# Kernel optimization log

Hardware: AMD Instinct MI355X
Metric: run time of the kernel (lower is better)

Reference implementation:

```python
import jax, jax.numpy as jnp
import numpy as np

IMG_W = 256; IMG_H = 256; N_PTS = 320
MIN_DEPTH = 3.0; MAX_DEPTH = 9.0
NDC_EXTENT = 1.0; SCALING = 0.1; EPS = 1e-10


def setup_inputs() -> dict:
    key = jax.random.key(0)
    k1, k2, k3 = jax.random.split(key, 3)
    B, S = 1, 256
    image3d = jax.random.uniform(k1, (B, 1, S, S, S), dtype=jnp.float32)
    # random proper rotation via QR
    A = jax.random.normal(k2, (B, 3, 3), dtype=jnp.float32)
    Q, _ = jnp.linalg.qr(A)
    det = jnp.linalg.det(Q)
    R = Q * det[:, None, None]  # det(+1) for 3x3
    # camera ~6 world units in front of volume center (depth range 3..9)
    T = jnp.concatenate([0.1 * jax.random.normal(k3, (B, 2), dtype=jnp.float32),
                         jnp.full((B, 1), 6.0, jnp.float32)], axis=1)
    focal = jnp.full((B,), 4.0, jnp.float32)
    return {"image3d": image3d, "R": R, "T": T, "focal": focal}


def _trilinear(vol, pts):
    # vol: (C,D,H,W); pts: (N,3) xyz local coords in [-1,1]
    # grid_sample semantics: trilinear, align_corners=True, zero padding
    C, D, H, W = vol.shape
    gx = (pts[:, 0] + 1.0) * 0.5 * (W - 1)
    gy = (pts[:, 1] + 1.0) * 0.5 * (H - 1)
    gz = (pts[:, 2] + 1.0) * 0.5 * (D - 1)
    x0 = jnp.floor(gx); y0 = jnp.floor(gy); z0 = jnp.floor(gz)
    fx = gx - x0; fy = gy - y0; fz = gz - z0
    vol_flat = vol.reshape(C, D * H * W)
    out = jnp.zeros((C, pts.shape[0]), vol.dtype)
    for dz in (0, 1):
        wz = fz if dz else 1.0 - fz
        cz = z0 + dz
        for dy in (0, 1):
            wy = fy if dy else 1.0 - fy
            cy = y0 + dy
            for dx in (0, 1):
                wx = fx if dx else 1.0 - fx
                cx = x0 + dx
                valid = ((cx >= 0) & (cx <= W - 1) & (cy >= 0) & (cy <= H - 1)
                         & (cz >= 0) & (cz <= D - 1)).astype(vol.dtype)
                idx = ((jnp.clip(cz, 0, D - 1) * H + jnp.clip(cy, 0, H - 1)) * W
                       + jnp.clip(cx, 0, W - 1)).astype(jnp.int32)
                w = wx * wy * wz * valid
                out = out + vol_flat[:, idx] * w[None, :]
    return out


def _render(image3d, R, T, focal):
    B, C, D, H, W = image3d.shape
    voxel_size = 2.0 * NDC_EXTENT / max(C, D)  # shape = max(C, D) in original
    # Volumes local<->world scale per axis (pytorch3d): voxel_size*(size-1)/2
    scale = jnp.array([voxel_size * (W - 1) / 2.0,
                       voxel_size * (H - 1) / 2.0,
                       voxel_size * (D - 1) / 2.0], jnp.float32)
    # NDCMultinomialRaysampler pixel grid (pytorch3d: +x left, +y up, decreasing)
    xs = jnp.linspace(1.0 - 1.0 / IMG_W, -1.0 + 1.0 / IMG_W, IMG_W)
    ys = jnp.linspace(1.0 - 1.0 / IMG_H, -1.0 + 1.0 / IMG_H, IMG_H)
    depths = jnp.linspace(MIN_DEPTH, MAX_DEPTH, N_PTS).astype(jnp.float32)
    gy, gx = jnp.meshgrid(ys, xs, indexing="ij")  # (Hi,Wi)

    # channel 0: gray volume (features); channel 1: ones (density support)
    vol2 = jnp.concatenate([image3d[:, :1], jnp.ones_like(image3d[:, :1])], axis=1)

    def one(volC, Rb, Tb, fb):
        # unproject NDC pixels at each depth: cam pt = (x*d/f, y*d/f, d)
        cx = gx[:, :, None] * depths[None, None, :] / fb
        cy = gy[:, :, None] * depths[None, None, :] / fb
        cz = jnp.broadcast_to(depths, (IMG_H, IMG_W, N_PTS))
        cam = jnp.stack([cx, cy, cz], -1).reshape(-1, 3)       # (N,3)
        world = (cam - Tb) @ Rb.T                              # X_view = X_world @ R + T
        local = world / scale
        return _trilinear(volC, local)                          # (2,N)

    samp = jax.vmap(one)(vol2, R, T, focal)                     # (B,2,N)
    samp = samp.reshape(B, 2, IMG_H, IMG_W, N_PTS)
    gray = samp[:, 0]
    dens = SCALING * samp[:, 1]

    # EmissionAbsorptionRaymarcher (shifted cumprod, shift=1)
    cp = jnp.cumprod((1.0 + EPS) - dens, axis=-1)
    absorption = jnp.concatenate([jnp.ones_like(cp[..., :1]), cp[..., :-1]], axis=-1)
    weights = dens * absorption
    feat = jnp.sum(weights * gray, axis=-1)                     # RGB channels are equal
    opacity = 1.0 - jnp.prod(1.0 - dens, axis=-1)

    # RGBA (B,Hi,Wi,4) -> permute(0,3,2,1) -> mean over channel = (3*feat+alpha)/4
    screen = (3.0 * feat + opacity) / 4.0
    screen = jnp.transpose(screen, (0, 2, 1))[:, None]          # (B,1,Wi,Hi)

    # norm_type='standardized': normalized(standardized(x)), torch std is unbiased
    s = (screen - screen.mean()) / (jnp.std(screen, ddof=1) + 1e-8)
    return (s - s.min() + 1e-8) / (s.max() - s.min() + 1e-8)


def reference(image3d, R, T, focal):
    return _render(image3d, R, T, focal)
```

## Files before the change

### kernel.cpp

```cpp
#include <hip/hip_runtime.h>
#include <math.h>

#define IMG    256
#define NPTS   320
#define CHUNKS 8
#define SPC    40
#define NBLK   1024

__global__ __launch_bounds__(512)
void xray_render(const float* __restrict__ vol,
                 const float* __restrict__ Rm,
                 const float* __restrict__ Tv,
                 const float* __restrict__ fc,
                 float* __restrict__ outv,
                 float* __restrict__ partials)
{
    const int tid = threadIdx.x;
    const int p   = tid & 63;
    const int c   = tid >> 6;
    const int w   = (blockIdx.x << 3) + (p & 7);
    const int h   = (blockIdx.y << 3) + (p >> 3);

    const float f   = fc[0];
    const float r00 = Rm[0], r01 = Rm[1], r02 = Rm[2];
    const float r10 = Rm[3], r11 = Rm[4], r12 = Rm[5];
    const float r20 = Rm[6], r21 = Rm[7], r22 = Rm[8];
    const float t0  = Tv[0], t1  = Tv[1], t2  = Tv[2];

    const float invf = 1.0f / f;
    const float px = 0.99609375f - (float)w * 0.0078125f;
    const float py = 0.99609375f - (float)h * 0.0078125f;
    const float dcx = px * invf, dcy = py * invf;

    const float dwx = r00*dcx + r01*dcy + r02;
    const float dwy = r10*dcx + r11*dcy + r12;
    const float dwz = r20*dcx + r21*dcy + r22;
    const float ox  = -(r00*t0 + r01*t1 + r02*t2);
    const float oy  = -(r10*t0 + r11*t1 + r12*t2);
    const float oz  = -(r20*t0 + r21*t1 + r22*t2);

    const float g0x = fmaf(384.0f, dwx, fmaf(128.0f, ox, 127.5f));
    const float g0y = fmaf(384.0f, dwy, fmaf(128.0f, oy, 127.5f));
    const float g0z = fmaf(384.0f, dwz, fmaf(128.0f, oz, 127.5f));
    const float K   = 768.0f / 319.0f;
    const float gsx = K*dwx, gsy = K*dwy, gsz = K*dwz;

    float raylo = -1e30f, rayhi = 1e30f;
    float inlo  = -1e30f, inhi  = 1e30f;
    {
        const float g0a[3] = {g0x, g0y, g0z};
        const float gsa[3] = {gsx, gsy, gsz};
        #pragma unroll
        for (int a = 0; a < 3; ++a) {
            const float g0 = g0a[a], gs = gsa[a];
            if (fabsf(gs) > 1e-6f) {
                const float r = 1.0f / gs;
                const float u = (-1.0f  - g0) * r;
                const float v = (256.0f - g0) * r;
                raylo = fmaxf(raylo, fminf(u, v));
                rayhi = fminf(rayhi, fmaxf(u, v));
                const float s = (0.001f   - g0) * r;
                const float t = (254.999f - g0) * r;
                inlo = fmaxf(inlo, fminf(s, t));
                inhi = fminf(inhi, fmaxf(s, t));
            } else {
                if (!(g0 > -1.0f && g0 < 256.0f))        { raylo = 1e30f; rayhi = -1e30f; }
                if (!(g0 > 0.001f && g0 < 254.999f))     { inlo  = 1e30f; inhi  = -1e30f; }
            }
        }
    }
    const float c0f = (float)(c * SPC);
    const float c1f = c0f + (float)(SPC - 1);
    float a0 = fminf(fmaxf(fmaxf(raylo - 1.0f, c0f), 0.0f),  400.0f);
    float a1 = fminf(fmaxf(fminf(rayhi + 1.0f, c1f), -1.0f), 400.0f);
    const int i0 = (int)ceilf(a0);
    const int i1 = (int)floorf(a1);
    float b0 = fminf(fmaxf(inlo, (float)i0), 401.0f);
    float b1 = fmaxf(fminf(inhi, (float)i1), -2.0f);
    const int jLo = (int)ceilf(b0);
    const int jHi = (int)floorf(b1);

    float feat = 0.0f, Tc = 1.0f;

    auto bstep = [&](int i) {
        const float fi = (float)i;
        const float gx = fmaf(fi, gsx, g0x);
        const float gy = fmaf(fi, gsy, g0y);
        const float gz = fmaf(fi, gsz, g0z);
        const float xf = floorf(gx), yf = floorf(gy), zf = floorf(gz);
        const float fx = gx - xf, fy = gy - yf, fz = gz - zf;
        const int ix = (int)xf, iy = (int)yf, iz = (int)zf;
        const float wx0 = (ix >= 0  && ix <= 255) ? (1.0f - fx) : 0.0f;
        const float wx1 = (ix >= -1 && ix <= 254) ? fx          : 0.0f;
        const float wy0 = (iy >= 0  && iy <= 255) ? (1.0f - fy) : 0.0f;
        const float wy1 = (iy >= -1 && iy <= 254) ? fy          : 0.0f;
        const float wz0 = (iz >= 0  && iz <= 255) ? (1.0f - fz) : 0.0f;
        const float wz1 = (iz >= -1 && iz <= 254) ? fz          : 0.0f;
        const float cov = (wx0 + wx1) * (wy0 + wy1) * (wz0 + wz1);
        if (cov > 0.0f) {
            const int x0 = min(max(ix, 0), 255),   x1 = min(max(ix + 1, 0), 255);
            const int y0 = min(max(iy, 0), 255),   y1 = min(max(iy + 1, 0), 255);
            const int z0 = min(max(iz, 0), 255),   z1 = min(max(iz + 1, 0), 255);
            const float* bz0 = vol + (z0 << 16);
            const float* bz1 = vol + (z1 << 16);
            const int ry0 = y0 << 8, ry1 = y1 << 8;
            const float s0 = (bz0[ry0 + x0]*wx0 + bz0[ry0 + x1]*wx1) * wy0
                           + (bz0[ry1 + x0]*wx0 + bz0[ry1 + x1]*wx1) * wy1;
            const float s1 = (bz1[ry0 + x0]*wx0 + bz1[ry0 + x1]*wx1) * wy0
                           + (bz1[ry1 + x0]*wx0 + bz1[ry1 + x1]*wx1) * wy1;
            const float gray = s0 * wz0 + s1 * wz1;
            const float dens = 0.1f * cov;
            feat = fmaf(dens * Tc, gray, feat);
            Tc *= (1.0f - dens);
        }
    };

    if (jLo <= jHi) {
        for (int i = i0; i < jLo; ++i) bstep(i);

        #pragma unroll 4
        for (int i = jLo; i <= jHi; ++i) {
            const float fi = (float)i;
            const float gx = fmaf(fi, gsx, g0x);
            const float gy = fmaf(fi, gsy, g0y);
            const float gz = fmaf(fi, gsz, g0z);
            const int ix = (int)gx;
            const int iy = (int)gy;
            const int iz = (int)gz;
            const float fx = gx - (float)ix;
            const float fy = gy - (float)iy;
            const float fz = gz - (float)iz;
            const float* b = vol + ((iz << 16) + (iy << 8) + ix);
            const float v000 = b[0],     v001 = b[1];
            const float v010 = b[256],   v011 = b[257];
            const float v100 = b[65536], v101 = b[65537];
            const float v110 = b[65792], v111 = b[65793];
            const float c00 = fmaf(fx, v001 - v000, v000);
            const float c01 = fmaf(fx, v011 - v010, v010);
            const float c10 = fmaf(fx, v101 - v100, v100);
            const float c11 = fmaf(fx, v111 - v110, v110);
            const float d0  = fmaf(fy, c01 - c00, c00);
            const float d1  = fmaf(fy, c11 - c10, c10);
            const float gray = fmaf(fz, d1 - d0, d0);
            feat = fmaf(0.1f * Tc, gray, feat);
            Tc *= 0.9f;
        }

        for (int i = jHi + 1; i <= i1; ++i) bstep(i);
    } else {
        for (int i = i0; i <= i1; ++i) bstep(i);
    }

    __shared__ float sf[CHUNKS][64];
    __shared__ float sT[CHUNKS][64];
    sf[c][p] = feat; sT[c][p] = Tc;
    __syncthreads();

    if (tid < 64) {
        float F = sf[CHUNKS - 1][p];
        #pragma unroll
        for (int j = CHUNKS - 2; j >= 0; --j) F = fmaf(sT[j][p], F, sf[j][p]);
        float PR = sT[0][p];
        #pragma unroll
        for (int j = 1; j < CHUNKS; ++j) PR *= sT[j][p];

        const float screen = fmaf(3.0f, F, 1.0f - PR) * 0.25f;
        outv[(w << 8) + h] = screen;

        float s = screen, s2 = screen * screen, mn = screen, mx = screen;
        #pragma unroll
        for (int o = 32; o; o >>= 1) {
            s  += __shfl_xor(s,  o);
            s2 += __shfl_xor(s2, o);
            mn  = fminf(mn, __shfl_xor(mn, o));
            mx  = fmaxf(mx, __shfl_xor(mx, o));
        }
        if (p == 0) {
            const int bid = (blockIdx.y << 5) + blockIdx.x;
            partials[bid * 4 + 0] = s;
            partials[bid * 4 + 1] = s2;
            partials[bid * 4 + 2] = mn;
            partials[bid * 4 + 3] = mx;
        }
    }
}

__global__ __launch_bounds__(256)
void xray_normalize(float* __restrict__ outv, const float* __restrict__ partials)
{
    const int t = threadIdx.x;
    double s = 0.0, s2 = 0.0;
    float mn = 1e30f, mx = -1e30f;
    #pragma unroll
    for (int j = 0; j < NBLK / 256; ++j) {
        const int idx = (j * 256 + t) * 4;
        s  += (double)partials[idx + 0];
        s2 += (double)partials[idx + 1];
        mn  = fminf(mn, partials[idx + 2]);
        mx  = fmaxf(mx, partials[idx + 3]);
    }
    #pragma unroll
    for (int o = 32; o; o >>= 1) {
        s  += __shfl_xor(s,  o);
        s2 += __shfl_xor(s2, o);
        mn  = fminf(mn, __shfl_xor(mn, o));
        mx  = fmaxf(mx, __shfl_xor(mx, o));
    }
    __shared__ double ls[4], ls2[4];
    __shared__ float  lmn[4], lmx[4];
    __shared__ float  soff, sinv;
    const int wid = t >> 6, lane = t & 63;
    if (lane == 0) { ls[wid] = s; ls2[wid] = s2; lmn[wid] = mn; lmx[wid] = mx; }
    __syncthreads();
    if (t == 0) {
        const double S  = ls[0] + ls[1] + ls[2] + ls[3];
        const double S2 = ls2[0] + ls2[1] + ls2[2] + ls2[3];
        const float MN = fminf(fminf(lmn[0], lmn[1]), fminf(lmn[2], lmn[3]));
        const float MX = fmaxf(fmaxf(lmx[0], lmx[1]), fmaxf(lmx[2], lmx[3]));
        double var = (S2 - S * S / 65536.0) / 65535.0;
        if (var < 0.0) var = 0.0;
        const double sdp = sqrt(var) + 1e-8;
        const float off = MN - (float)(1e-8 * sdp);
        soff = off;
        sinv = 1.0f / (MX - off);
    }
    __syncthreads();
    const int i = blockIdx.x * 256 + t;
    outv[i] = (outv[i] - soff) * sinv;
}

extern "C" void kernel_launch(void* const* d_in, const int* in_sizes, int n_in,
                              void* d_out, int out_size, void* d_ws, size_t ws_size,
                              hipStream_t stream)
{
    const float* vol = (const float*)d_in[0];
    const float* Rm  = (const float*)d_in[1];
    const float* Tv  = (const float*)d_in[2];
    const float* fc  = (const float*)d_in[3];
    float* outv = (float*)d_out;
    float* partials = (float*)d_ws;

    dim3 grid(IMG / 8, IMG / 8);
    xray_render<<<grid, 512, 0, stream>>>(vol, Rm, Tv, fc, outv, partials);
    xray_normalize<<<IMG * IMG / 256, 256, 0, stream>>>(outv, partials);
}
```

Measured before the change: 73.61 us.

## Split rays into more chunks with smaller tiles and batch paired voxel loads

Each ray is now split into 16 chunks of 20 samples, and blocks become 4x4-pixel tiles of 256 threads, giving four times as many blocks for better occupancy and load balance. The interior sampling loop is hand-unrolled by four so that all gathers are issued before any arithmetic, and adjacent x-voxels are fetched as 8-byte pairs to halve the load instruction count. Partials are written and read as float4. In exchange, the partials buffer grows, the normalize reduction does more work, and the 8-byte loads may be unaligned.

```diff
diff --git a/kernel.cpp b/kernel.cpp
--- a/kernel.cpp
+++ b/kernel.cpp
@@ -3,11 +3,16 @@
 
 #define IMG    256
 #define NPTS   320
-#define CHUNKS 8
-#define SPC    40
-#define NBLK   1024
-
-__global__ __launch_bounds__(512)
+#define CHUNKS 16
+#define SPC    20
+#define NBLK   4096
+
+struct f2 { float lo, hi; };
+__device__ __forceinline__ f2 ld2(const float* p) {
+    f2 r; __builtin_memcpy(&r, p, 8); return r;
+}
+
+__global__ __launch_bounds__(256)
 void xray_render(const float* __restrict__ vol,
                  const float* __restrict__ Rm,
                  const float* __restrict__ Tv,
@@ -16,10 +21,10 @@
                  float* __restrict__ partials)
 {
     const int tid = threadIdx.x;
-    const int p   = tid & 63;
-    const int c   = tid >> 6;
-    const int w   = (blockIdx.x << 3) + (p & 7);
-    const int h   = (blockIdx.y << 3) + (p >> 3);
+    const int p   = tid & 15;
+    const int c   = tid >> 4;
+    const int w   = (blockIdx.x << 2) + (p & 3);
+    const int h   = (blockIdx.y << 2) + (p >> 2);
 
     const float f   = fc[0];
     const float r00 = Rm[0], r01 = Rm[1], r02 = Rm[2];
@@ -115,48 +120,84 @@
         }
     };
 
+    auto istep = [&](int i) {
+        const float fi = (float)i;
+        const float gx = fmaf(fi, gsx, g0x);
+        const float gy = fmaf(fi, gsy, g0y);
+        const float gz = fmaf(fi, gsz, g0z);
+        const int ix = (int)gx, iy = (int)gy, iz = (int)gz;
+        const float fx = gx - (float)ix;
+        const float fy = gy - (float)iy;
+        const float fz = gz - (float)iz;
+        const float* b = vol + ((iz << 16) + (iy << 8) + ix);
+        const f2 a00 = ld2(b);
+        const f2 a01 = ld2(b + 256);
+        const f2 a10 = ld2(b + 65536);
+        const f2 a11 = ld2(b + 65792);
+        const float c00 = fmaf(fx, a00.hi - a00.lo, a00.lo);
+        const float c01 = fmaf(fx, a01.hi - a01.lo, a01.lo);
+        const float c10 = fmaf(fx, a10.hi - a10.lo, a10.lo);
+        const float c11 = fmaf(fx, a11.hi - a11.lo, a11.lo);
+        const float d0  = fmaf(fy, c01 - c00, c00);
+        const float d1  = fmaf(fy, c11 - c10, c10);
+        const float gray = fmaf(fz, d1 - d0, d0);
+        feat = fmaf(0.1f * Tc, gray, feat);
+        Tc *= 0.9f;
+    };
+
     if (jLo <= jHi) {
         for (int i = i0; i < jLo; ++i) bstep(i);
 
-        #pragma unroll 4
-        for (int i = jLo; i <= jHi; ++i) {
-            const float fi = (float)i;
-            const float gx = fmaf(fi, gsx, g0x);
-            const float gy = fmaf(fi, gsy, g0y);
-            const float gz = fmaf(fi, gsz, g0z);
-            const int ix = (int)gx;
-            const int iy = (int)gy;
-            const int iz = (int)gz;
-            const float fx = gx - (float)ix;
-            const float fy = gy - (float)iy;
-            const float fz = gz - (float)iz;
-            const float* b = vol + ((iz << 16) + (iy << 8) + ix);
-            const float v000 = b[0],     v001 = b[1];
-            const float v010 = b[256],   v011 = b[257];
-            const float v100 = b[65536], v101 = b[65537];
-            const float v110 = b[65792], v111 = b[65793];
-            const float c00 = fmaf(fx, v001 - v000, v000);
-            const float c01 = fmaf(fx, v011 - v010, v010);
-            const float c10 = fmaf(fx, v101 - v100, v100);
-            const float c11 = fmaf(fx, v111 - v110, v110);
-            const float d0  = fmaf(fy, c01 - c00, c00);
-            const float d1  = fmaf(fy, c11 - c10, c10);
-            const float gray = fmaf(fz, d1 - d0, d0);
-            feat = fmaf(0.1f * Tc, gray, feat);
-            Tc *= 0.9f;
-        }
+        int i = jLo;
+        for (; i + 3 <= jHi; i += 4) {
+            float fx[4], fy[4], fz[4];
+            const float* bp[4];
+            #pragma unroll
+            for (int k = 0; k < 4; ++k) {
+                const float fi = (float)(i + k);
+                const float gx = fmaf(fi, gsx, g0x);
+                const float gy = fmaf(fi, gsy, g0y);
+                const float gz = fmaf(fi, gsz, g0z);
+                const int ix = (int)gx, iy = (int)gy, iz = (int)gz;
+                fx[k] = gx - (float)ix;
+                fy[k] = gy - (float)iy;
+                fz[k] = gz - (float)iz;
+                bp[k] = vol + ((iz << 16) + (iy << 8) + ix);
+            }
+            f2 a00[4], a01[4], a10[4], a11[4];
+            #pragma unroll
+            for (int k = 0; k < 4; ++k) {
+                a00[k] = ld2(bp[k]);
+                a01[k] = ld2(bp[k] + 256);
+                a10[k] = ld2(bp[k] + 65536);
+                a11[k] = ld2(bp[k] + 65792);
+            }
+            #pragma unroll
+            for (int k = 0; k < 4; ++k) {
+                const float c00 = fmaf(fx[k], a00[k].hi - a00[k].lo, a00[k].lo);
+                const float c01 = fmaf(fx[k], a01[k].hi - a01[k].lo, a01[k].lo);
+                const float c10 = fmaf(fx[k], a10[k].hi - a10[k].lo, a10[k].lo);
+                const float c11 = fmaf(fx[k], a11[k].hi - a11[k].lo, a11[k].lo);
+                const float d0  = fmaf(fy[k], c01 - c00, c00);
+                const float d1  = fmaf(fy[k], c11 - c10, c10);
+                const float gray = fmaf(fz[k], d1 - d0, d0);
+                feat = fmaf(0.1f * Tc, gray, feat);
+                Tc *= 0.9f;
+            }
+        }
+        for (; i <= jHi; ++i) istep(i);
 
         for (int i = jHi + 1; i <= i1; ++i) bstep(i);
     } else {
         for (int i = i0; i <= i1; ++i) bstep(i);
     }
 
-    __shared__ float sf[CHUNKS][64];
-    __shared__ float sT[CHUNKS][64];
+    __shared__ float sf[CHUNKS][16];
+    __shared__ float sT[CHUNKS][16];
     sf[c][p] = feat; sT[c][p] = Tc;
     __syncthreads();
 
-    if (tid < 64) {
+    if (tid < 16) {
         float F = sf[CHUNKS - 1][p];
         #pragma unroll
         for (int j = CHUNKS - 2; j >= 0; --j) F = fmaf(sT[j][p], F, sf[j][p]);
@@ -169,18 +210,16 @@
 
         float s = screen, s2 = screen * screen, mn = screen, mx = screen;
         #pragma unroll
-        for (int o = 32; o; o >>= 1) {
+        for (int o = 8; o; o >>= 1) {
             s  += __shfl_xor(s,  o);
             s2 += __shfl_xor(s2, o);
             mn  = fminf(mn, __shfl_xor(mn, o));
             mx  = fmaxf(mx, __shfl_xor(mx, o));
         }
         if (p == 0) {
-            const int bid = (blockIdx.y << 5) + blockIdx.x;
-            partials[bid * 4 + 0] = s;
-            partials[bid * 4 + 1] = s2;
-            partials[bid * 4 + 2] = mn;
-            partials[bid * 4 + 3] = mx;
+            const int bid = (blockIdx.y << 6) + blockIdx.x;
+            float4* out4 = (float4*)partials;
+            out4[bid] = make_float4(s, s2, mn, mx);
         }
     }
 }
@@ -189,15 +228,16 @@
 void xray_normalize(float* __restrict__ outv, const float* __restrict__ partials)
 {
     const int t = threadIdx.x;
+    const float4* p4 = (const float4*)partials;
     double s = 0.0, s2 = 0.0;
     float mn = 1e30f, mx = -1e30f;
     #pragma unroll
     for (int j = 0; j < NBLK / 256; ++j) {
-        const int idx = (j * 256 + t) * 4;
-        s  += (double)partials[idx + 0];
-        s2 += (double)partials[idx + 1];
-        mn  = fminf(mn, partials[idx + 2]);
-        mx  = fmaxf(mx, partials[idx + 3]);
+        const float4 v = p4[j * 256 + t];
+        s  += (double)v.x;
+        s2 += (double)v.y;
+        mn  = fminf(mn, v.z);
+        mx  = fmaxf(mx, v.w);
     }
     #pragma unroll
     for (int o = 32; o; o >>= 1) {
@@ -240,7 +280,7 @@
     float* outv = (float*)d_out;
     float* partials = (float*)d_ws;
 
-    dim3 grid(IMG / 8, IMG / 8);
-    xray_render<<<grid, 512, 0, stream>>>(vol, Rm, Tv, fc, outv, partials);
+    dim3 grid(IMG / 4, IMG / 4);
+    xray_render<<<grid, 256, 0, stream>>>(vol, Rm, Tv, fc, outv, partials);
     xray_normalize<<<IMG * IMG / 256, 256, 0, stream>>>(outv, partials);
 }
```

Result: slower. 81.75 us (+11.0%).
